# Optimization experiments

Hardware: AMD Instinct MI355X
Metric: run time of the kernel (lower is better)

Reference implementation:

```python
import jax, jax.numpy as jnp
import numpy as np
import math

D_MODEL = 1024
NUM_HEADS = 16
BATCH = 2
SEQ = 2048

def setup_inputs() -> dict:
    key = jax.random.key(0)
    ks = jax.random.split(key, 9)
    s = 1.0 / math.sqrt(D_MODEL)
    inp = {
        "X": jax.random.normal(ks[0], (BATCH, SEQ, D_MODEL), dtype=jnp.float32),
        "Wq": jax.random.uniform(ks[1], (D_MODEL, D_MODEL), jnp.float32, -s, s),
        "bq": jax.random.uniform(ks[2], (D_MODEL,), jnp.float32, -s, s),
        "Wk": jax.random.uniform(ks[3], (D_MODEL, D_MODEL), jnp.float32, -s, s),
        "bk": jax.random.uniform(ks[4], (D_MODEL,), jnp.float32, -s, s),
        "Wv": jax.random.uniform(ks[5], (D_MODEL, D_MODEL), jnp.float32, -s, s),
        "bv": jax.random.uniform(ks[6], (D_MODEL,), jnp.float32, -s, s),
        "Wo": jax.random.uniform(ks[7], (D_MODEL, D_MODEL), jnp.float32, -s, s),
        "bo": jax.random.uniform(ks[8], (D_MODEL,), jnp.float32, -s, s),
    }
    return inp

def reference(X, Wq, bq, Wk, bk, Wv, bv, Wo, bo):
    B, S, D = X.shape
    H = NUM_HEADS
    dk = D // H
    # QKV projections (Linear: x @ W.T + b; here W stored as [in, out] so x @ W + b)
    q = X @ Wq + bq
    k = X @ Wk + bk
    v = X @ Wv + bv
    # split heads -> [B, H, S, dk]
    q = q.reshape(B, S, H, dk).transpose(0, 2, 1, 3)
    k = k.reshape(B, S, H, dk).transpose(0, 2, 1, 3)
    v = v.reshape(B, S, H, dk).transpose(0, 2, 1, 3)
    scores = jnp.einsum("bhqd,bhkd->bhqk", q, k) / math.sqrt(dk)
    weights = jax.nn.softmax(scores, axis=-1)
    attn = jnp.einsum("bhqk,bhkd->bhqd", weights, v)
    concat = attn.transpose(0, 2, 1, 3).reshape(B, S, D)
    return concat @ Wo + bo
```

## Files before the change

kernel.cpp:

```cpp
#include <hip/hip_runtime.h>
#include <stdint.h>

#define D_MODEL 1024
#define NH      16
#define DKH     64
#define BATCH   2
#define SEQ     2048
#define M_TOK   (BATCH*SEQ)

typedef __attribute__((ext_vector_type(8))) short bf16x8;
typedef __attribute__((ext_vector_type(4))) float f32x4;

__device__ __forceinline__ uint16_t f2b(float f) {
  uint32_t u = __builtin_bit_cast(uint32_t, f);
  return (uint16_t)((u + 0x7FFFu + ((u >> 16) & 1u)) >> 16);
}

__device__ __forceinline__ void gl2lds16(const uint16_t* g, uint16_t* l) {
  __builtin_amdgcn_global_load_lds(
      (const __attribute__((address_space(1))) void*)g,
      (__attribute__((address_space(3))) void*)l, 16, 0, 0);
}

__global__ void convx(const float* __restrict__ X, uint16_t* __restrict__ Xb) {
  int i = (blockIdx.x * 256 + threadIdx.x) * 8;
  float4 a = *(const float4*)(X + i);
  float4 b = *(const float4*)(X + i + 4);
  uint16_t tmp[8] = {f2b(a.x), f2b(a.y), f2b(a.z), f2b(a.w),
                     f2b(b.x), f2b(b.y), f2b(b.z), f2b(b.w)};
  *(uint4*)(Xb + i) = *(const uint4*)tmp;
}

__global__ void wtrans(const float* __restrict__ W0, const float* __restrict__ W1,
                       const float* __restrict__ W2, const float* __restrict__ W3,
                       uint16_t* __restrict__ T0, uint16_t* __restrict__ T1,
                       uint16_t* __restrict__ T2, uint16_t* __restrict__ T3) {
  __shared__ float tile[32][33];
  int z = blockIdx.z;
  const float* W = (z == 0) ? W0 : (z == 1) ? W1 : (z == 2) ? W2 : W3;
  uint16_t*    T = (z == 0) ? T0 : (z == 1) ? T1 : (z == 2) ? T2 : T3;
  int k0 = blockIdx.x * 32, n0 = blockIdx.y * 32;
  int tx = threadIdx.x, ty = threadIdx.y;
  tile[ty][tx] = W[(size_t)(k0 + ty) * D_MODEL + n0 + tx];
  __syncthreads();
  T[(size_t)(n0 + ty) * D_MODEL + k0 + tx] = f2b(tile[tx][ty]);
}

template <bool SWAP>
__device__ __forceinline__ void gemm_core(const uint16_t* __restrict__ A,
                                          const uint16_t* __restrict__ BT,
                                          uint16_t* As, uint16_t* Bs,
                                          int m0, int n0, int kBeg, int kEnd,
                                          f32x4 (&acc)[4][4]) {
  const int t    = threadIdx.x;
  const int lane = t & 63;
  const int qi   = lane & 15, g = lane >> 4;
  const int wm   = (t >> 7) & 1;
  const int wn   = (t >> 6) & 1;
  const int srow = t >> 2;
  const int sc   = (t & 3) ^ ((t >> 3) & 3);
  const int wbase = t & 192;
  const int rch  = (g ^ ((qi >> 1) & 3)) * 8;

  const uint16_t* Ag = A  + (size_t)(m0 + srow) * D_MODEL + sc * 8;
  const uint16_t* Bg = BT + (size_t)(n0 + srow) * D_MODEL + sc * 8;

#pragma unroll
  for (int j = 0; j < 2; j++) {
    gl2lds16(Ag + (size_t)j * 64 * D_MODEL + kBeg, As + (j * 256 + wbase) * 8);
    gl2lds16(Bg + (size_t)j * 64 * D_MODEL + kBeg, Bs + (j * 256 + wbase) * 8);
  }

  int cur = 0;
  for (int k0 = kBeg; k0 < kEnd; k0 += 32) {
    __syncthreads();
    int kn = k0 + 32;
    if (kn < kEnd) {
      int nb = (cur ^ 1) * 4096;
#pragma unroll
      for (int j = 0; j < 2; j++) {
        gl2lds16(Ag + (size_t)j * 64 * D_MODEL + kn, As + nb + (j * 256 + wbase) * 8);
        gl2lds16(Bg + (size_t)j * 64 * D_MODEL + kn, Bs + nb + (j * 256 + wbase) * 8);
      }
    }
    const uint16_t* Ab = As + cur * 4096;
    const uint16_t* Bb = Bs + cur * 4096;
    bf16x8 af[4], bf[4];
#pragma unroll
    for (int i = 0; i < 4; i++) {
      af[i] = *(const bf16x8*)(Ab + (wm * 64 + i * 16 + qi) * 32 + rch);
      bf[i] = *(const bf16x8*)(Bb + (wn * 64 + i * 16 + qi) * 32 + rch);
    }
#pragma unroll
    for (int i = 0; i < 4; i++)
#pragma unroll
      for (int j = 0; j < 4; j++)
        acc[i][j] = SWAP
          ? __builtin_amdgcn_mfma_f32_16x16x32_bf16(bf[j], af[i], acc[i][j], 0, 0, 0)
          : __builtin_amdgcn_mfma_f32_16x16x32_bf16(af[i], bf[j], acc[i][j], 0, 0, 0);
    cur ^= 1;
  }
}

__global__ __launch_bounds__(256) void qkv_gemm(
    const uint16_t* __restrict__ Xb,
    const uint16_t* __restrict__ WqT, const uint16_t* __restrict__ WkT,
    const uint16_t* __restrict__ WvT,
    const float* __restrict__ bq, const float* __restrict__ bk,
    const float* __restrict__ bv,
    uint16_t* __restrict__ Qo, uint16_t* __restrict__ Ko, uint16_t* __restrict__ Vt) {
  __shared__ __align__(16) uint16_t smem[17408];
  uint16_t* As = smem;
  uint16_t* Bs = smem + 8192;
  uint16_t* T  = smem;
  const int z = blockIdx.z;
  const uint16_t* BT  = (z == 0) ? WqT : (z == 1) ? WkT : WvT;
  const float*   bias = (z == 0) ? bq  : (z == 1) ? bk  : bv;
  const int m0 = blockIdx.y * 128, n0 = blockIdx.x * 128;
  const int lane = threadIdx.x & 63, qi = lane & 15, g = lane >> 4;
  const int wm = (threadIdx.x >> 7) & 1, wn = (threadIdx.x >> 6) & 1;
  const float l2e = 1.4426950408889634f * 0.125f;

  const f32x4 ZERO = {0.f, 0.f, 0.f, 0.f};
  f32x4 acc[4][4];
#pragma unroll
  for (int i = 0; i < 4; i++)
#pragma unroll
    for (int j = 0; j < 4; j++) acc[i][j] = ZERO;

  if (z == 2) {
    gemm_core<false>(Xb, BT, As, Bs, m0, n0, 0, D_MODEL, acc);
    __syncthreads();
#pragma unroll
    for (int i = 0; i < 4; i++) {
      int tok = wm * 64 + i * 16 + g * 4;
#pragma unroll
      for (int j = 0; j < 4; j++) {
        int ch = wn * 64 + j * 16 + qi;
        float bb = bias[n0 + ch];
        uint32_t lo = (uint32_t)f2b(acc[i][j][0] + bb) | ((uint32_t)f2b(acc[i][j][1] + bb) << 16);
        uint32_t hi = (uint32_t)f2b(acc[i][j][2] + bb) | ((uint32_t)f2b(acc[i][j][3] + bb) << 16);
        uint2 pk = {lo, hi};
        *(uint2*)(T + ch * 136 + tok) = pk;
      }
    }
    __syncthreads();
    {
      int ch = threadIdx.x >> 1, sh = threadIdx.x & 1;
      const uint16_t* src = T + ch * 136 + sh * 64;
      int bidx = m0 >> 11;
      uint16_t* dst = Vt + ((size_t)(bidx * D_MODEL + n0 + ch)) * SEQ + (m0 & 2047) + sh * 64;
#pragma unroll
      for (int u = 0; u < 8; u++)
        *(uint4*)(dst + u * 8) = *(const uint4*)(src + u * 8);
    }
  } else {
    gemm_core<true>(Xb, BT, As, Bs, m0, n0, 0, D_MODEL, acc);
    uint16_t* O = z ? Ko : Qo;
    const float osc = (z == 0) ? l2e : 1.0f;
#pragma unroll
    for (int i = 0; i < 4; i++) {
      size_t tok = m0 + wm * 64 + i * 16 + qi;
#pragma unroll
      for (int j = 0; j < 4; j++) {
        int ch = n0 + wn * 64 + j * 16 + g * 4;
        float4 bb = *(const float4*)(bias + ch);
        uint32_t lo = (uint32_t)f2b((acc[i][j][0] + bb.x) * osc) |
                      ((uint32_t)f2b((acc[i][j][1] + bb.y) * osc) << 16);
        uint32_t hi = (uint32_t)f2b((acc[i][j][2] + bb.z) * osc) |
                      ((uint32_t)f2b((acc[i][j][3] + bb.w) * osc) << 16);
        uint2 pk = {lo, hi};
        *(uint2*)(O + tok * D_MODEL + ch) = pk;
      }
    }
  }
}

__global__ __launch_bounds__(256) void oproj_gemm(
    const uint16_t* __restrict__ Ab, const uint16_t* __restrict__ WoT,
    const float* __restrict__ bo, float* __restrict__ out) {
  __shared__ __align__(16) uint16_t As[8192];
  __shared__ __align__(16) uint16_t Bs[4096];
  const int t = threadIdx.x;
  const int lane = t & 63, qi = lane & 15, g = lane >> 4;
  const int wm = (t >> 7) & 1;
  const int wn = (t >> 6) & 1;
  const int srow = t >> 2;
  const int sc = (t & 3) ^ ((t >> 3) & 3);
  const int wbase = t & 192;
  const int rch = (g ^ ((qi >> 1) & 3)) * 8;
  const int m0 = blockIdx.y * 128, n0 = blockIdx.x * 64;

  const uint16_t* Ag = Ab  + (size_t)(m0 + srow) * D_MODEL + sc * 8;
  const uint16_t* Bg = WoT + (size_t)(n0 + srow) * D_MODEL + sc * 8;

  const f32x4 ZERO = {0.f, 0.f, 0.f, 0.f};
  f32x4 acc[4][2];
#pragma unroll
  for (int i = 0; i < 4; i++)
#pragma unroll
    for (int j = 0; j < 2; j++) acc[i][j] = ZERO;

  gl2lds16(Ag, As + wbase * 8);
  gl2lds16(Ag + (size_t)64 * D_MODEL, As + (256 + wbase) * 8);
  gl2lds16(Bg, Bs + wbase * 8);

  int cur = 0;
  for (int k0 = 0; k0 < D_MODEL; k0 += 32) {
    __syncthreads();
    int kn = k0 + 32;
    if (kn < D_MODEL) {
      int nbA = (cur ^ 1) * 4096, nbB = (cur ^ 1) * 2048;
      gl2lds16(Ag + kn, As + nbA + wbase * 8);
      gl2lds16(Ag + (size_t)64 * D_MODEL + kn, As + nbA + (256 + wbase) * 8);
      gl2lds16(Bg + kn, Bs + nbB + wbase * 8);
    }
    const uint16_t* Abuf = As + cur * 4096;
    const uint16_t* Bbuf = Bs + cur * 2048;
    bf16x8 af[4], bf[2];
#pragma unroll
    for (int i = 0; i < 4; i++)
      af[i] = *(const bf16x8*)(Abuf + (wm * 64 + i * 16 + qi) * 32 + rch);
#pragma unroll
    for (int j = 0; j < 2; j++)
      bf[j] = *(const bf16x8*)(Bbuf + (wn * 32 + j * 16 + qi) * 32 + rch);
#pragma unroll
    for (int i = 0; i < 4; i++)
#pragma unroll
      for (int j = 0; j < 2; j++)
        acc[i][j] = __builtin_amdgcn_mfma_f32_16x16x32_bf16(bf[j], af[i], acc[i][j], 0, 0, 0);
    cur ^= 1;
  }

#pragma unroll
  for (int i = 0; i < 4; i++) {
    size_t tok = m0 + wm * 64 + i * 16 + qi;
#pragma unroll
    for (int j = 0; j < 2; j++) {
      int ch = n0 + wn * 32 + j * 16 + g * 4;
      float4 bb = *(const float4*)(bo + ch);
      float4 o = {acc[i][j][0] + bb.x, acc[i][j][1] + bb.y,
                  acc[i][j][2] + bb.z, acc[i][j][3] + bb.w};
      *(float4*)(out + tok * D_MODEL + ch) = o;
    }
  }
}

__global__ __launch_bounds__(256) void attn_fwd(
    const uint16_t* __restrict__ Q, const uint16_t* __restrict__ K,
    const uint16_t* __restrict__ Vt, uint16_t* __restrict__ O) {
  __shared__ __align__(16) uint16_t sm[24576];
  uint16_t* Ps = sm + 16384;

  const int t = threadIdx.x, lane = t & 63, w = t >> 6;
  const int g = lane >> 4, qi = lane & 15;
  const int wbase = t & 192;
  const int sc = (t & 3) ^ ((t >> 3) & 3);
  const int rch = (g ^ ((qi >> 1) & 3)) * 8;
  const int key = qi & 7;
  const int q0 = blockIdx.x * 128;
  const int bh = blockIdx.y, b = bh >> 4, h = bh & 15;
  const uint16_t* Qp = Q + (size_t)b * SEQ * D_MODEL + h * DKH;
  const uint16_t* Kp = K + (size_t)b * SEQ * D_MODEL + h * DKH;
  const uint16_t* Vp = Vt + (size_t)bh * DKH * SEQ;

  const int srow = t >> 2, c8 = sc * 8;

#pragma unroll
  for (int hs = 0; hs < 2; hs++)
#pragma unroll
    for (int j = 0; j < 2; j++)
      gl2lds16(Qp + (size_t)(q0 + j * 64 + srow) * D_MODEL + hs * 32 + c8,
               sm + 16384 + hs * 4096 + (j * 256 + wbase) * 8);
  {
    const uint16_t* Kr = Kp + (size_t)srow * D_MODEL;
    const uint16_t* Vr = Vp + (size_t)srow * SEQ;
    gl2lds16(Kr + c8,      sm + wbase * 8);
    gl2lds16(Kr + 32 + c8, sm + 2048 + wbase * 8);
    gl2lds16(Vr + c8,      sm + 8192 + wbase * 8);
    gl2lds16(Vr + 32 + c8, sm + 8192 + 2048 + wbase * 8);
  }
  __syncthreads();

  bf16x8 qf[2][2];
#pragma unroll
  for (int ks = 0; ks < 2; ks++)
#pragma unroll
    for (int i = 0; i < 2; i++)
      qf[ks][i] = *(const bf16x8*)(sm + 16384 + ks * 4096 + (w * 32 + i * 16 + qi) * 32 + rch);
  __syncthreads();

  float lsum[2] = {0.f, 0.f};
  const f32x4 ZERO = {0.f, 0.f, 0.f, 0.f};
  f32x4 oaccT[4][2];
#pragma unroll
  for (int d = 0; d < 4; d++)
#pragma unroll
    for (int i = 0; i < 2; i++) oaccT[d][i] = ZERO;

  int cur = 0;
  for (int kt = 0; kt < SEQ / 64; kt++) {
    if (kt + 1 < SEQ / 64) {
      int nb = (cur ^ 1) * 4096;
      const uint16_t* Kr = Kp + (size_t)((kt + 1) * 64 + srow) * D_MODEL;
      const uint16_t* Vr = Vp + (size_t)srow * SEQ + (kt + 1) * 64;
      gl2lds16(Kr + c8,      sm + nb + wbase * 8);
      gl2lds16(Kr + 32 + c8, sm + nb + 2048 + wbase * 8);
      gl2lds16(Vr + c8,      sm + 8192 + nb + wbase * 8);
      gl2lds16(Vr + 32 + c8, sm + 8192 + nb + 2048 + wbase * 8);
    }
    const uint16_t* Kb = sm + cur * 4096;
    const uint16_t* Vb = sm + 8192 + cur * 4096;

    f32x4 sacc[4][2];
#pragma unroll
    for (int j = 0; j < 4; j++)
#pragma unroll
      for (int i = 0; i < 2; i++) sacc[j][i] = ZERO;
#pragma unroll
    for (int ks = 0; ks < 2; ks++) {
      const uint16_t* Ksb = Kb + ks * 2048;
      bf16x8 kf[4];
#pragma unroll
      for (int j = 0; j < 4; j++)
        kf[j] = *(const bf16x8*)(Ksb + (j * 16 + qi) * 32 + rch);
#pragma unroll
      for (int j = 0; j < 4; j++)
#pragma unroll
        for (int i = 0; i < 2; i++)
          sacc[j][i] = __builtin_amdgcn_mfma_f32_16x16x32_bf16(kf[j], qf[ks][i], sacc[j][i], 0, 0, 0);
    }

#pragma unroll
    for (int i = 0; i < 2; i++) {
      uint16_t* Pr = Ps + (w * 32 + i * 16 + qi) * 64;
#pragma unroll
      for (int j = 0; j < 4; j++) {
        float p0 = __builtin_amdgcn_exp2f(sacc[j][i][0]);
        float p1 = __builtin_amdgcn_exp2f(sacc[j][i][1]);
        float p2 = __builtin_amdgcn_exp2f(sacc[j][i][2]);
        float p3 = __builtin_amdgcn_exp2f(sacc[j][i][3]);
        lsum[i] += (p0 + p1) + (p2 + p3);
        uint2 pk = {__builtin_amdgcn_perm(__builtin_bit_cast(uint32_t, p1),
                                          __builtin_bit_cast(uint32_t, p0), 0x07060302u),
                    __builtin_amdgcn_perm(__builtin_bit_cast(uint32_t, p3),
                                          __builtin_bit_cast(uint32_t, p2), 0x07060302u)};
        *(uint2*)(Pr + (((j * 4 + g) ^ (2 * key)) << 2)) = pk;
      }
    }

#pragma unroll
    for (int ks = 0; ks < 2; ks++) {
      const uint16_t* Vsb = Vb + ks * 2048;
      bf16x8 vf[4], pf[2];
#pragma unroll
      for (int d = 0; d < 4; d++)
        vf[d] = *(const bf16x8*)(Vsb + (d * 16 + qi) * 32 + rch);
#pragma unroll
      for (int i = 0; i < 2; i++)
        pf[i] = *(const bf16x8*)(Ps + (w * 32 + i * 16 + qi) * 64 +
                                 (((ks * 4 + g) ^ key) << 3));
#pragma unroll
      for (int d = 0; d < 4; d++)
#pragma unroll
        for (int i = 0; i < 2; i++)
          oaccT[d][i] = __builtin_amdgcn_mfma_f32_16x16x32_bf16(vf[d], pf[i], oaccT[d][i], 0, 0, 0);
    }

    if (kt + 1 < SEQ / 64) __syncthreads();
    cur ^= 1;
  }

#pragma unroll
  for (int i = 0; i < 2; i++) {
    lsum[i] += __shfl_xor(lsum[i], 16, 64);
    lsum[i] += __shfl_xor(lsum[i], 32, 64);
  }
  float rl[2] = {1.f / lsum[0], 1.f / lsum[1]};

#pragma unroll
  for (int i = 0; i < 2; i++) {
    size_t row = (size_t)b * SEQ + q0 + w * 32 + i * 16 + qi;
#pragma unroll
    for (int d = 0; d < 4; d++) {
      uint32_t lo = (uint32_t)f2b(oaccT[d][i][0] * rl[i]) |
                    ((uint32_t)f2b(oaccT[d][i][1] * rl[i]) << 16);
      uint32_t hi = (uint32_t)f2b(oaccT[d][i][2] * rl[i]) |
                    ((uint32_t)f2b(oaccT[d][i][3] * rl[i]) << 16);
      uint2 pk = {lo, hi};
      *(uint2*)(O + row * D_MODEL + h * DKH + d * 16 + g * 4) = pk;
    }
  }
}

extern "C" void kernel_launch(void* const* d_in, const int* in_sizes, int n_in,
                              void* d_out, int out_size, void* d_ws, size_t ws_size,
                              hipStream_t stream) {
  (void)in_sizes; (void)n_in; (void)out_size; (void)ws_size;
  const float* X  = (const float*)d_in[0];
  const float* Wq = (const float*)d_in[1];
  const float* bq = (const float*)d_in[2];
  const float* Wk = (const float*)d_in[3];
  const float* bk = (const float*)d_in[4];
  const float* Wv = (const float*)d_in[5];
  const float* bv = (const float*)d_in[6];
  const float* Wo = (const float*)d_in[7];
  const float* bo = (const float*)d_in[8];
  float* out = (float*)d_out;

  char* p = (char*)d_ws;
  uint16_t* Xb  = (uint16_t*)p; p += (size_t)M_TOK * D_MODEL * 2;
  uint16_t* WqT = (uint16_t*)p; p += (size_t)D_MODEL * D_MODEL * 2;
  uint16_t* WkT = (uint16_t*)p; p += (size_t)D_MODEL * D_MODEL * 2;
  uint16_t* WvT = (uint16_t*)p; p += (size_t)D_MODEL * D_MODEL * 2;
  uint16_t* WoT = (uint16_t*)p; p += (size_t)D_MODEL * D_MODEL * 2;
  uint16_t* Qw  = (uint16_t*)p; p += (size_t)M_TOK * D_MODEL * 2;
  uint16_t* Kw  = (uint16_t*)p; p += (size_t)M_TOK * D_MODEL * 2;
  uint16_t* Vt  = (uint16_t*)p; p += (size_t)M_TOK * D_MODEL * 2;
  uint16_t* Ob  = (uint16_t*)p; p += (size_t)M_TOK * D_MODEL * 2;

  convx<<<(M_TOK * D_MODEL) / (256 * 8), 256, 0, stream>>>(X, Xb);
  wtrans<<<dim3(32, 32, 4), dim3(32, 32), 0, stream>>>(Wq, Wk, Wv, Wo, WqT, WkT, WvT, WoT);
  qkv_gemm<<<dim3(8, 32, 3), 256, 0, stream>>>(Xb, WqT, WkT, WvT, bq, bk, bv, Qw, Kw, Vt);
  attn_fwd<<<dim3(SEQ / 128, BATCH * NH), 256, 0, stream>>>(Qw, Kw, Vt, Ob);
  oproj_gemm<<<dim3(16, 32), 256, 0, stream>>>(Ob, WoT, bo, out);
}
```

Before: 203.9 us.

## Split attention over key halves with combine kernel; narrow QKV GEMM tiles

Attention is split into two key-range halves along a new grid dimension. Each half writes unnormalized fp32 partial outputs and row sums, and a new combine kernel adds them, normalizes and writes bf16. The QKV GEMM switches to a shared 128x64 tile routine, doubling its block count. This raises parallelism and occupancy, at the cost of extra fp32 partial traffic, an added launch, and reliance on the softmax not needing per-split max rescaling.

```diff
diff --git a/kernel.cpp b/kernel.cpp
--- a/kernel.cpp
+++ b/kernel.cpp
@@ -47,11 +47,10 @@
 }
 
 template <bool SWAP>
-__device__ __forceinline__ void gemm_core(const uint16_t* __restrict__ A,
-                                          const uint16_t* __restrict__ BT,
-                                          uint16_t* As, uint16_t* Bs,
-                                          int m0, int n0, int kBeg, int kEnd,
-                                          f32x4 (&acc)[4][4]) {
+__device__ __forceinline__ void gemm64(const uint16_t* __restrict__ A,
+                                       const uint16_t* __restrict__ BT,
+                                       uint16_t* As, uint16_t* Bs,
+                                       int m0, int n0, f32x4 (&acc)[4][2]) {
   const int t    = threadIdx.x;
   const int lane = t & 63;
   const int qi   = lane & 15, g = lane >> 4;
@@ -65,142 +64,6 @@
   const uint16_t* Ag = A  + (size_t)(m0 + srow) * D_MODEL + sc * 8;
   const uint16_t* Bg = BT + (size_t)(n0 + srow) * D_MODEL + sc * 8;
 
-#pragma unroll
-  for (int j = 0; j < 2; j++) {
-    gl2lds16(Ag + (size_t)j * 64 * D_MODEL + kBeg, As + (j * 256 + wbase) * 8);
-    gl2lds16(Bg + (size_t)j * 64 * D_MODEL + kBeg, Bs + (j * 256 + wbase) * 8);
-  }
-
-  int cur = 0;
-  for (int k0 = kBeg; k0 < kEnd; k0 += 32) {
-    __syncthreads();
-    int kn = k0 + 32;
-    if (kn < kEnd) {
-      int nb = (cur ^ 1) * 4096;
-#pragma unroll
-      for (int j = 0; j < 2; j++) {
-        gl2lds16(Ag + (size_t)j * 64 * D_MODEL + kn, As + nb + (j * 256 + wbase) * 8);
-        gl2lds16(Bg + (size_t)j * 64 * D_MODEL + kn, Bs + nb + (j * 256 + wbase) * 8);
-      }
-    }
-    const uint16_t* Ab = As + cur * 4096;
-    const uint16_t* Bb = Bs + cur * 4096;
-    bf16x8 af[4], bf[4];
-#pragma unroll
-    for (int i = 0; i < 4; i++) {
-      af[i] = *(const bf16x8*)(Ab + (wm * 64 + i * 16 + qi) * 32 + rch);
-      bf[i] = *(const bf16x8*)(Bb + (wn * 64 + i * 16 + qi) * 32 + rch);
-    }
-#pragma unroll
-    for (int i = 0; i < 4; i++)
-#pragma unroll
-      for (int j = 0; j < 4; j++)
-        acc[i][j] = SWAP
-          ? __builtin_amdgcn_mfma_f32_16x16x32_bf16(bf[j], af[i], acc[i][j], 0, 0, 0)
-          : __builtin_amdgcn_mfma_f32_16x16x32_bf16(af[i], bf[j], acc[i][j], 0, 0, 0);
-    cur ^= 1;
-  }
-}
-
-__global__ __launch_bounds__(256) void qkv_gemm(
-    const uint16_t* __restrict__ Xb,
-    const uint16_t* __restrict__ WqT, const uint16_t* __restrict__ WkT,
-    const uint16_t* __restrict__ WvT,
-    const float* __restrict__ bq, const float* __restrict__ bk,
-    const float* __restrict__ bv,
-    uint16_t* __restrict__ Qo, uint16_t* __restrict__ Ko, uint16_t* __restrict__ Vt) {
-  __shared__ __align__(16) uint16_t smem[17408];
-  uint16_t* As = smem;
-  uint16_t* Bs = smem + 8192;
-  uint16_t* T  = smem;
-  const int z = blockIdx.z;
-  const uint16_t* BT  = (z == 0) ? WqT : (z == 1) ? WkT : WvT;
-  const float*   bias = (z == 0) ? bq  : (z == 1) ? bk  : bv;
-  const int m0 = blockIdx.y * 128, n0 = blockIdx.x * 128;
-  const int lane = threadIdx.x & 63, qi = lane & 15, g = lane >> 4;
-  const int wm = (threadIdx.x >> 7) & 1, wn = (threadIdx.x >> 6) & 1;
-  const float l2e = 1.4426950408889634f * 0.125f;
-
-  const f32x4 ZERO = {0.f, 0.f, 0.f, 0.f};
-  f32x4 acc[4][4];
-#pragma unroll
-  for (int i = 0; i < 4; i++)
-#pragma unroll
-    for (int j = 0; j < 4; j++) acc[i][j] = ZERO;
-
-  if (z == 2) {
-    gemm_core<false>(Xb, BT, As, Bs, m0, n0, 0, D_MODEL, acc);
-    __syncthreads();
-#pragma unroll
-    for (int i = 0; i < 4; i++) {
-      int tok = wm * 64 + i * 16 + g * 4;
-#pragma unroll
-      for (int j = 0; j < 4; j++) {
-        int ch = wn * 64 + j * 16 + qi;
-        float bb = bias[n0 + ch];
-        uint32_t lo = (uint32_t)f2b(acc[i][j][0] + bb) | ((uint32_t)f2b(acc[i][j][1] + bb) << 16);
-        uint32_t hi = (uint32_t)f2b(acc[i][j][2] + bb) | ((uint32_t)f2b(acc[i][j][3] + bb) << 16);
-        uint2 pk = {lo, hi};
-        *(uint2*)(T + ch * 136 + tok) = pk;
-      }
-    }
-    __syncthreads();
-    {
-      int ch = threadIdx.x >> 1, sh = threadIdx.x & 1;
-      const uint16_t* src = T + ch * 136 + sh * 64;
-      int bidx = m0 >> 11;
-      uint16_t* dst = Vt + ((size_t)(bidx * D_MODEL + n0 + ch)) * SEQ + (m0 & 2047) + sh * 64;
-#pragma unroll
-      for (int u = 0; u < 8; u++)
-        *(uint4*)(dst + u * 8) = *(const uint4*)(src + u * 8);
-    }
-  } else {
-    gemm_core<true>(Xb, BT, As, Bs, m0, n0, 0, D_MODEL, acc);
-    uint16_t* O = z ? Ko : Qo;
-    const float osc = (z == 0) ? l2e : 1.0f;
-#pragma unroll
-    for (int i = 0; i < 4; i++) {
-      size_t tok = m0 + wm * 64 + i * 16 + qi;
-#pragma unroll
-      for (int j = 0; j < 4; j++) {
-        int ch = n0 + wn * 64 + j * 16 + g * 4;
-        float4 bb = *(const float4*)(bias + ch);
-        uint32_t lo = (uint32_t)f2b((acc[i][j][0] + bb.x) * osc) |
-                      ((uint32_t)f2b((acc[i][j][1] + bb.y) * osc) << 16);
-        uint32_t hi = (uint32_t)f2b((acc[i][j][2] + bb.z) * osc) |
-                      ((uint32_t)f2b((acc[i][j][3] + bb.w) * osc) << 16);
-        uint2 pk = {lo, hi};
-        *(uint2*)(O + tok * D_MODEL + ch) = pk;
-      }
-    }
-  }
-}
-
-__global__ __launch_bounds__(256) void oproj_gemm(
-    const uint16_t* __restrict__ Ab, const uint16_t* __restrict__ WoT,
-    const float* __restrict__ bo, float* __restrict__ out) {
-  __shared__ __align__(16) uint16_t As[8192];
-  __shared__ __align__(16) uint16_t Bs[4096];
-  const int t = threadIdx.x;
-  const int lane = t & 63, qi = lane & 15, g = lane >> 4;
-  const int wm = (t >> 7) & 1;
-  const int wn = (t >> 6) & 1;
-  const int srow = t >> 2;
-  const int sc = (t & 3) ^ ((t >> 3) & 3);
-  const int wbase = t & 192;
-  const int rch = (g ^ ((qi >> 1) & 3)) * 8;
-  const int m0 = blockIdx.y * 128, n0 = blockIdx.x * 64;
-
-  const uint16_t* Ag = Ab  + (size_t)(m0 + srow) * D_MODEL + sc * 8;
-  const uint16_t* Bg = WoT + (size_t)(n0 + srow) * D_MODEL + sc * 8;
-
-  const f32x4 ZERO = {0.f, 0.f, 0.f, 0.f};
-  f32x4 acc[4][2];
-#pragma unroll
-  for (int i = 0; i < 4; i++)
-#pragma unroll
-    for (int j = 0; j < 2; j++) acc[i][j] = ZERO;
-
   gl2lds16(Ag, As + wbase * 8);
   gl2lds16(Ag + (size_t)64 * D_MODEL, As + (256 + wbase) * 8);
   gl2lds16(Bg, Bs + wbase * 8);
@@ -215,22 +78,116 @@
       gl2lds16(Ag + (size_t)64 * D_MODEL + kn, As + nbA + (256 + wbase) * 8);
       gl2lds16(Bg + kn, Bs + nbB + wbase * 8);
     }
-    const uint16_t* Abuf = As + cur * 4096;
-    const uint16_t* Bbuf = Bs + cur * 2048;
+    const uint16_t* Ab = As + cur * 4096;
+    const uint16_t* Bb = Bs + cur * 2048;
     bf16x8 af[4], bf[2];
 #pragma unroll
     for (int i = 0; i < 4; i++)
-      af[i] = *(const bf16x8*)(Abuf + (wm * 64 + i * 16 + qi) * 32 + rch);
+      af[i] = *(const bf16x8*)(Ab + (wm * 64 + i * 16 + qi) * 32 + rch);
 #pragma unroll
     for (int j = 0; j < 2; j++)
-      bf[j] = *(const bf16x8*)(Bbuf + (wn * 32 + j * 16 + qi) * 32 + rch);
+      bf[j] = *(const bf16x8*)(Bb + (wn * 32 + j * 16 + qi) * 32 + rch);
 #pragma unroll
     for (int i = 0; i < 4; i++)
 #pragma unroll
       for (int j = 0; j < 2; j++)
-        acc[i][j] = __builtin_amdgcn_mfma_f32_16x16x32_bf16(bf[j], af[i], acc[i][j], 0, 0, 0);
+        acc[i][j] = SWAP
+          ? __builtin_amdgcn_mfma_f32_16x16x32_bf16(bf[j], af[i], acc[i][j], 0, 0, 0)
+          : __builtin_amdgcn_mfma_f32_16x16x32_bf16(af[i], bf[j], acc[i][j], 0, 0, 0);
     cur ^= 1;
   }
+}
+
+__global__ __launch_bounds__(256) void qkv_gemm(
+    const uint16_t* __restrict__ Xb,
+    const uint16_t* __restrict__ WqT, const uint16_t* __restrict__ WkT,
+    const uint16_t* __restrict__ WvT,
+    const float* __restrict__ bq, const float* __restrict__ bk,
+    const float* __restrict__ bv,
+    uint16_t* __restrict__ Qo, uint16_t* __restrict__ Ko, uint16_t* __restrict__ Vt) {
+  __shared__ __align__(16) uint16_t smem[12288];
+  uint16_t* As = smem;
+  uint16_t* Bs = smem + 8192;
+  uint16_t* T  = smem;
+  const int z = blockIdx.z;
+  const uint16_t* BT  = (z == 0) ? WqT : (z == 1) ? WkT : WvT;
+  const float*   bias = (z == 0) ? bq  : (z == 1) ? bk  : bv;
+  const int m0 = blockIdx.y * 128, n0 = blockIdx.x * 64;
+  const int lane = threadIdx.x & 63, qi = lane & 15, g = lane >> 4;
+  const int wm = (threadIdx.x >> 7) & 1, wn = (threadIdx.x >> 6) & 1;
+  const float l2e = 1.4426950408889634f * 0.125f;
+
+  const f32x4 ZERO = {0.f, 0.f, 0.f, 0.f};
+  f32x4 acc[4][2];
+#pragma unroll
+  for (int i = 0; i < 4; i++)
+#pragma unroll
+    for (int j = 0; j < 2; j++) acc[i][j] = ZERO;
+
+  if (z == 2) {
+    gemm64<false>(Xb, BT, As, Bs, m0, n0, acc);
+    __syncthreads();
+#pragma unroll
+    for (int i = 0; i < 4; i++) {
+      int tok = wm * 64 + i * 16 + g * 4;
+#pragma unroll
+      for (int j = 0; j < 2; j++) {
+        int ch = wn * 32 + j * 16 + qi;
+        float bb = bias[n0 + ch];
+        uint32_t lo = (uint32_t)f2b(acc[i][j][0] + bb) | ((uint32_t)f2b(acc[i][j][1] + bb) << 16);
+        uint32_t hi = (uint32_t)f2b(acc[i][j][2] + bb) | ((uint32_t)f2b(acc[i][j][3] + bb) << 16);
+        uint2 pk = {lo, hi};
+        *(uint2*)(T + ch * 136 + tok) = pk;
+      }
+    }
+    __syncthreads();
+    {
+      int ch = threadIdx.x >> 2, sh = threadIdx.x & 3;
+      const uint16_t* src = T + ch * 136 + sh * 32;
+      int bidx = m0 >> 11;
+      uint16_t* dst = Vt + ((size_t)(bidx * D_MODEL + n0 + ch)) * SEQ + (m0 & 2047) + sh * 32;
+#pragma unroll
+      for (int u = 0; u < 4; u++)
+        *(uint4*)(dst + u * 8) = *(const uint4*)(src + u * 8);
+    }
+  } else {
+    gemm64<true>(Xb, BT, As, Bs, m0, n0, acc);
+    uint16_t* O = z ? Ko : Qo;
+    const float osc = (z == 0) ? l2e : 1.0f;
+#pragma unroll
+    for (int i = 0; i < 4; i++) {
+      size_t tok = m0 + wm * 64 + i * 16 + qi;
+#pragma unroll
+      for (int j = 0; j < 2; j++) {
+        int ch = n0 + wn * 32 + j * 16 + g * 4;
+        float4 bb = *(const float4*)(bias + ch);
+        uint32_t lo = (uint32_t)f2b((acc[i][j][0] + bb.x) * osc) |
+                      ((uint32_t)f2b((acc[i][j][1] + bb.y) * osc) << 16);
+        uint32_t hi = (uint32_t)f2b((acc[i][j][2] + bb.z) * osc) |
+                      ((uint32_t)f2b((acc[i][j][3] + bb.w) * osc) << 16);
+        uint2 pk = {lo, hi};
+        *(uint2*)(O + tok * D_MODEL + ch) = pk;
+      }
+    }
+  }
+}
+
+__global__ __launch_bounds__(256) void oproj_gemm(
+    const uint16_t* __restrict__ Ab, const uint16_t* __restrict__ WoT,
+    const float* __restrict__ bo, float* __restrict__ out) {
+  __shared__ __align__(16) uint16_t As[8192];
+  __shared__ __align__(16) uint16_t Bs[4096];
+  const int m0 = blockIdx.y * 128, n0 = blockIdx.x * 64;
+  const int lane = threadIdx.x & 63, qi = lane & 15, g = lane >> 4;
+  const int wm = (threadIdx.x >> 7) & 1, wn = (threadIdx.x >> 6) & 1;
+  const f32x4 ZERO = {0.f, 0.f, 0.f, 0.f};
+  f32x4 acc[4][2];
+#pragma unroll
+  for (int i = 0; i < 4; i++)
+#pragma unroll
+    for (int j = 0; j < 2; j++) acc[i][j] = ZERO;
+
+  gemm64<true>(Ab, WoT, As, Bs, m0, n0, acc);
 
 #pragma unroll
   for (int i = 0; i < 4; i++) {
@@ -248,7 +205,8 @@
 
 __global__ __launch_bounds__(256) void attn_fwd(
     const uint16_t* __restrict__ Q, const uint16_t* __restrict__ K,
-    const uint16_t* __restrict__ Vt, uint16_t* __restrict__ O) {
+    const uint16_t* __restrict__ Vt,
+    float* __restrict__ P0, float* __restrict__ P1, float* __restrict__ lw) {
   __shared__ __align__(16) uint16_t sm[24576];
   uint16_t* Ps = sm + 16384;
 
@@ -258,8 +216,10 @@
   const int sc = (t & 3) ^ ((t >> 3) & 3);
   const int rch = (g ^ ((qi >> 1) & 3)) * 8;
   const int key = qi & 7;
-  const int q0 = blockIdx.x * 128;
+  const int qt = blockIdx.x, q0 = qt * 128;
   const int bh = blockIdx.y, b = bh >> 4, h = bh & 15;
+  const int kz = blockIdx.z;
+  const int ktBeg = kz * 16, ktEnd = ktBeg + 16;
   const uint16_t* Qp = Q + (size_t)b * SEQ * D_MODEL + h * DKH;
   const uint16_t* Kp = K + (size_t)b * SEQ * D_MODEL + h * DKH;
   const uint16_t* Vp = Vt + (size_t)bh * DKH * SEQ;
@@ -273,8 +233,8 @@
       gl2lds16(Qp + (size_t)(q0 + j * 64 + srow) * D_MODEL + hs * 32 + c8,
                sm + 16384 + hs * 4096 + (j * 256 + wbase) * 8);
   {
-    const uint16_t* Kr = Kp + (size_t)srow * D_MODEL;
-    const uint16_t* Vr = Vp + (size_t)srow * SEQ;
+    const uint16_t* Kr = Kp + (size_t)(ktBeg * 64 + srow) * D_MODEL;
+    const uint16_t* Vr = Vp + (size_t)srow * SEQ + ktBeg * 64;
     gl2lds16(Kr + c8,      sm + wbase * 8);
     gl2lds16(Kr + 32 + c8, sm + 2048 + wbase * 8);
     gl2lds16(Vr + c8,      sm + 8192 + wbase * 8);
@@ -299,8 +259,8 @@
     for (int i = 0; i < 2; i++) oaccT[d][i] = ZERO;
 
   int cur = 0;
-  for (int kt = 0; kt < SEQ / 64; kt++) {
-    if (kt + 1 < SEQ / 64) {
+  for (int kt = ktBeg; kt < ktEnd; kt++) {
+    if (kt + 1 < ktEnd) {
       int nb = (cur ^ 1) * 4096;
       const uint16_t* Kr = Kp + (size_t)((kt + 1) * 64 + srow) * D_MODEL;
       const uint16_t* Vr = Vp + (size_t)srow * SEQ + (kt + 1) * 64;
@@ -367,7 +327,7 @@
           oaccT[d][i] = __builtin_amdgcn_mfma_f32_16x16x32_bf16(vf[d], pf[i], oaccT[d][i], 0, 0, 0);
     }
 
-    if (kt + 1 < SEQ / 64) __syncthreads();
+    if (kt + 1 < ktEnd) __syncthreads();
     cur ^= 1;
   }
 
@@ -376,20 +336,42 @@
     lsum[i] += __shfl_xor(lsum[i], 16, 64);
     lsum[i] += __shfl_xor(lsum[i], 32, 64);
   }
-  float rl[2] = {1.f / lsum[0], 1.f / lsum[1]};
-
+  if (lane < 16) {
+    float* lp = lw + ((size_t)kz * 512 + bh * 16 + qt) * 128;
+#pragma unroll
+    for (int i = 0; i < 2; i++) lp[w * 32 + i * 16 + qi] = lsum[i];
+  }
+
+  float* Pout = (kz ? P1 : P0) + ((size_t)(bh * 16 + qt) * 128) * 64;
 #pragma unroll
   for (int i = 0; i < 2; i++) {
-    size_t row = (size_t)b * SEQ + q0 + w * 32 + i * 16 + qi;
-#pragma unroll
-    for (int d = 0; d < 4; d++) {
-      uint32_t lo = (uint32_t)f2b(oaccT[d][i][0] * rl[i]) |
-                    ((uint32_t)f2b(oaccT[d][i][1] * rl[i]) << 16);
-      uint32_t hi = (uint32_t)f2b(oaccT[d][i][2] * rl[i]) |
-                    ((uint32_t)f2b(oaccT[d][i][3] * rl[i]) << 16);
-      uint2 pk = {lo, hi};
-      *(uint2*)(O + row * D_MODEL + h * DKH + d * 16 + g * 4) = pk;
-    }
+    int q = w * 32 + i * 16 + qi;
+#pragma unroll
+    for (int d = 0; d < 4; d++)
+      *(f32x4*)(Pout + q * 64 + d * 16 + g * 4) = oaccT[d][i];
+  }
+}
+
+__global__ __launch_bounds__(256) void attn_combine(
+    const float* __restrict__ P0, const float* __restrict__ P1,
+    const float* __restrict__ lw, uint16_t* __restrict__ Ob) {
+  const int c = blockIdx.x;
+  const int bh = c >> 4, qt = c & 15;
+  const int b = bh >> 4, h = bh & 15;
+  const int t = threadIdx.x;
+  const int q = t >> 1, dh = (t & 1) * 32;
+  const float l = lw[(size_t)c * 128 + q] + lw[65536 + (size_t)c * 128 + q];
+  const float rl = 1.f / l;
+  const size_t base = ((size_t)c * 128 + q) * 64 + dh;
+  uint16_t* dst = Ob + ((size_t)(b * SEQ + qt * 128 + q)) * D_MODEL + h * DKH + dh;
+#pragma unroll
+  for (int u = 0; u < 8; u++) {
+    float4 a = *(const float4*)(P0 + base + u * 4);
+    float4 v = *(const float4*)(P1 + base + u * 4);
+    uint32_t lo = (uint32_t)f2b((a.x + v.x) * rl) | ((uint32_t)f2b((a.y + v.y) * rl) << 16);
+    uint32_t hi = (uint32_t)f2b((a.z + v.z) * rl) | ((uint32_t)f2b((a.w + v.w) * rl) << 16);
+    uint2 pk = {lo, hi};
+    *(uint2*)(dst + u * 4) = pk;
   }
 }
 
@@ -418,10 +400,14 @@
   uint16_t* Kw  = (uint16_t*)p; p += (size_t)M_TOK * D_MODEL * 2;
   uint16_t* Vt  = (uint16_t*)p; p += (size_t)M_TOK * D_MODEL * 2;
   uint16_t* Ob  = (uint16_t*)p; p += (size_t)M_TOK * D_MODEL * 2;
+  float*    P1  = (float*)p;    p += (size_t)M_TOK * D_MODEL * 4;
+  float*    lw  = (float*)p;    p += (size_t)2 * M_TOK * NH * 4;
+  float*    P0  = out;
 
   convx<<<(M_TOK * D_MODEL) / (256 * 8), 256, 0, stream>>>(X, Xb);
   wtrans<<<dim3(32, 32, 4), dim3(32, 32), 0, stream>>>(Wq, Wk, Wv, Wo, WqT, WkT, WvT, WoT);
-  qkv_gemm<<<dim3(8, 32, 3), 256, 0, stream>>>(Xb, WqT, WkT, WvT, bq, bk, bv, Qw, Kw, Vt);
-  attn_fwd<<<dim3(SEQ / 128, BATCH * NH), 256, 0, stream>>>(Qw, Kw, Vt, Ob);
+  qkv_gemm<<<dim3(16, 32, 3), 256, 0, stream>>>(Xb, WqT, WkT, WvT, bq, bk, bv, Qw, Kw, Vt);
+  attn_fwd<<<dim3(16, 32, 2), 256, 0, stream>>>(Qw, Kw, Vt, P0, P1, lw);
+  attn_combine<<<512, 256, 0, stream>>>(P0, P1, lw, Ob);
   oproj_gemm<<<dim3(16, 32), 256, 0, stream>>>(Ob, WoT, bo, out);
 }
```

Measured after the change: 232.4 us. 1.14x slower.

## Halve attention query tile to 64 rows and load Q straight into registers

Applied to the files above, without the earlier changes.

Each attention block now handles 64 queries instead of 128, with every wave owning 16 query rows, so the grid has twice as many blocks. Launch bounds are raised to 4 blocks per CU and the LDS footprint is trimmed. Q fragments are read from global memory directly into registers instead of being staged through LDS, which removes one barrier. The GEMM helpers are also refactored to drop unused k-range parameters and share an oproj core. The aim is better CU occupancy and latency hiding, at the cost of reading each K/V tile twice as often and getting less MFMA reuse per LDS load.

```diff
diff --git a/kernel.cpp b/kernel.cpp
--- a/kernel.cpp
+++ b/kernel.cpp
@@ -50,8 +50,7 @@
 __device__ __forceinline__ void gemm_core(const uint16_t* __restrict__ A,
                                           const uint16_t* __restrict__ BT,
                                           uint16_t* As, uint16_t* Bs,
-                                          int m0, int n0, int kBeg, int kEnd,
-                                          f32x4 (&acc)[4][4]) {
+                                          int m0, int n0, f32x4 (&acc)[4][4]) {
   const int t    = threadIdx.x;
   const int lane = t & 63;
   const int qi   = lane & 15, g = lane >> 4;
@@ -67,15 +66,15 @@
 
 #pragma unroll
   for (int j = 0; j < 2; j++) {
-    gl2lds16(Ag + (size_t)j * 64 * D_MODEL + kBeg, As + (j * 256 + wbase) * 8);
-    gl2lds16(Bg + (size_t)j * 64 * D_MODEL + kBeg, Bs + (j * 256 + wbase) * 8);
+    gl2lds16(Ag + (size_t)j * 64 * D_MODEL, As + (j * 256 + wbase) * 8);
+    gl2lds16(Bg + (size_t)j * 64 * D_MODEL, Bs + (j * 256 + wbase) * 8);
   }
 
   int cur = 0;
-  for (int k0 = kBeg; k0 < kEnd; k0 += 32) {
+  for (int k0 = 0; k0 < D_MODEL; k0 += 32) {
     __syncthreads();
     int kn = k0 + 32;
-    if (kn < kEnd) {
+    if (kn < D_MODEL) {
       int nb = (cur ^ 1) * 4096;
 #pragma unroll
       for (int j = 0; j < 2; j++) {
@@ -98,6 +97,55 @@
         acc[i][j] = SWAP
           ? __builtin_amdgcn_mfma_f32_16x16x32_bf16(bf[j], af[i], acc[i][j], 0, 0, 0)
           : __builtin_amdgcn_mfma_f32_16x16x32_bf16(af[i], bf[j], acc[i][j], 0, 0, 0);
+    cur ^= 1;
+  }
+}
+
+__device__ __forceinline__ void gemm64(const uint16_t* __restrict__ A,
+                                       const uint16_t* __restrict__ BT,
+                                       uint16_t* As, uint16_t* Bs,
+                                       int m0, int n0, f32x4 (&acc)[4][2]) {
+  const int t    = threadIdx.x;
+  const int lane = t & 63;
+  const int qi   = lane & 15, g = lane >> 4;
+  const int wm   = (t >> 7) & 1;
+  const int wn   = (t >> 6) & 1;
+  const int srow = t >> 2;
+  const int sc   = (t & 3) ^ ((t >> 3) & 3);
+  const int wbase = t & 192;
+  const int rch  = (g ^ ((qi >> 1) & 3)) * 8;
+
+  const uint16_t* Ag = A  + (size_t)(m0 + srow) * D_MODEL + sc * 8;
+  const uint16_t* Bg = BT + (size_t)(n0 + srow) * D_MODEL + sc * 8;
+
+  gl2lds16(Ag, As + wbase * 8);
+  gl2lds16(Ag + (size_t)64 * D_MODEL, As + (256 + wbase) * 8);
+  gl2lds16(Bg, Bs + wbase * 8);
+
+  int cur = 0;
+  for (int k0 = 0; k0 < D_MODEL; k0 += 32) {
+    __syncthreads();
+    int kn = k0 + 32;
+    if (kn < D_MODEL) {
+      int nbA = (cur ^ 1) * 4096, nbB = (cur ^ 1) * 2048;
+      gl2lds16(Ag + kn, As + nbA + wbase * 8);
+      gl2lds16(Ag + (size_t)64 * D_MODEL + kn, As + nbA + (256 + wbase) * 8);
+      gl2lds16(Bg + kn, Bs + nbB + wbase * 8);
+    }
+    const uint16_t* Ab = As + cur * 4096;
+    const uint16_t* Bb = Bs + cur * 2048;
+    bf16x8 af[4], bf[2];
+#pragma unroll
+    for (int i = 0; i < 4; i++)
+      af[i] = *(const bf16x8*)(Ab + (wm * 64 + i * 16 + qi) * 32 + rch);
+#pragma unroll
+    for (int j = 0; j < 2; j++)
+      bf[j] = *(const bf16x8*)(Bb + (wn * 32 + j * 16 + qi) * 32 + rch);
+#pragma unroll
+    for (int i = 0; i < 4; i++)
+#pragma unroll
+      for (int j = 0; j < 2; j++)
+        acc[i][j] = __builtin_amdgcn_mfma_f32_16x16x32_bf16(bf[j], af[i], acc[i][j], 0, 0, 0);
     cur ^= 1;
   }
 }
@@ -129,7 +177,7 @@
     for (int j = 0; j < 4; j++) acc[i][j] = ZERO;
 
   if (z == 2) {
-    gemm_core<false>(Xb, BT, As, Bs, m0, n0, 0, D_MODEL, acc);
+    gemm_core<false>(Xb, BT, As, Bs, m0, n0, acc);
     __syncthreads();
 #pragma unroll
     for (int i = 0; i < 4; i++) {
@@ -155,7 +203,7 @@
         *(uint4*)(dst + u * 8) = *(const uint4*)(src + u * 8);
     }
   } else {
-    gemm_core<true>(Xb, BT, As, Bs, m0, n0, 0, D_MODEL, acc);
+    gemm_core<true>(Xb, BT, As, Bs, m0, n0, acc);
     uint16_t* O = z ? Ko : Qo;
     const float osc = (z == 0) ? l2e : 1.0f;
 #pragma unroll
@@ -181,19 +229,9 @@
     const float* __restrict__ bo, float* __restrict__ out) {
   __shared__ __align__(16) uint16_t As[8192];
   __shared__ __align__(16) uint16_t Bs[4096];
-  const int t = threadIdx.x;
-  const int lane = t & 63, qi = lane & 15, g = lane >> 4;
-  const int wm = (t >> 7) & 1;
-  const int wn = (t >> 6) & 1;
-  const int srow = t >> 2;
-  const int sc = (t & 3) ^ ((t >> 3) & 3);
-  const int wbase = t & 192;
-  const int rch = (g ^ ((qi >> 1) & 3)) * 8;
   const int m0 = blockIdx.y * 128, n0 = blockIdx.x * 64;
-
-  const uint16_t* Ag = Ab  + (size_t)(m0 + srow) * D_MODEL + sc * 8;
-  const uint16_t* Bg = WoT + (size_t)(n0 + srow) * D_MODEL + sc * 8;
-
+  const int lane = threadIdx.x & 63, qi = lane & 15, g = lane >> 4;
+  const int wm = (threadIdx.x >> 7) & 1, wn = (threadIdx.x >> 6) & 1;
   const f32x4 ZERO = {0.f, 0.f, 0.f, 0.f};
   f32x4 acc[4][2];
 #pragma unroll
@@ -201,36 +239,7 @@
 #pragma unroll
     for (int j = 0; j < 2; j++) acc[i][j] = ZERO;
 
-  gl2lds16(Ag, As + wbase * 8);
-  gl2lds16(Ag + (size_t)64 * D_MODEL, As + (256 + wbase) * 8);
-  gl2lds16(Bg, Bs + wbase * 8);
-
-  int cur = 0;
-  for (int k0 = 0; k0 < D_MODEL; k0 += 32) {
-    __syncthreads();
-    int kn = k0 + 32;
-    if (kn < D_MODEL) {
-      int nbA = (cur ^ 1) * 4096, nbB = (cur ^ 1) * 2048;
-      gl2lds16(Ag + kn, As + nbA + wbase * 8);
-      gl2lds16(Ag + (size_t)64 * D_MODEL + kn, As + nbA + (256 + wbase) * 8);
-      gl2lds16(Bg + kn, Bs + nbB + wbase * 8);
-    }
-    const uint16_t* Abuf = As + cur * 4096;
-    const uint16_t* Bbuf = Bs + cur * 2048;
-    bf16x8 af[4], bf[2];
-#pragma unroll
-    for (int i = 0; i < 4; i++)
-      af[i] = *(const bf16x8*)(Abuf + (wm * 64 + i * 16 + qi) * 32 + rch);
-#pragma unroll
-    for (int j = 0; j < 2; j++)
-      bf[j] = *(const bf16x8*)(Bbuf + (wn * 32 + j * 16 + qi) * 32 + rch);
-#pragma unroll
-    for (int i = 0; i < 4; i++)
-#pragma unroll
-      for (int j = 0; j < 2; j++)
-        acc[i][j] = __builtin_amdgcn_mfma_f32_16x16x32_bf16(bf[j], af[i], acc[i][j], 0, 0, 0);
-    cur ^= 1;
-  }
+  gemm64(Ab, WoT, As, Bs, m0, n0, acc);
 
 #pragma unroll
   for (int i = 0; i < 4; i++) {
@@ -246,10 +255,10 @@
   }
 }
 
-__global__ __launch_bounds__(256) void attn_fwd(
+__global__ __launch_bounds__(256, 4) void attn_fwd(
     const uint16_t* __restrict__ Q, const uint16_t* __restrict__ K,
     const uint16_t* __restrict__ Vt, uint16_t* __restrict__ O) {
-  __shared__ __align__(16) uint16_t sm[24576];
+  __shared__ __align__(16) uint16_t sm[20480];
   uint16_t* Ps = sm + 16384;
 
   const int t = threadIdx.x, lane = t & 63, w = t >> 6;
@@ -258,20 +267,13 @@
   const int sc = (t & 3) ^ ((t >> 3) & 3);
   const int rch = (g ^ ((qi >> 1) & 3)) * 8;
   const int key = qi & 7;
-  const int q0 = blockIdx.x * 128;
+  const int q0 = blockIdx.x * 64;
   const int bh = blockIdx.y, b = bh >> 4, h = bh & 15;
   const uint16_t* Qp = Q + (size_t)b * SEQ * D_MODEL + h * DKH;
   const uint16_t* Kp = K + (size_t)b * SEQ * D_MODEL + h * DKH;
   const uint16_t* Vp = Vt + (size_t)bh * DKH * SEQ;
-
   const int srow = t >> 2, c8 = sc * 8;
 
-#pragma unroll
-  for (int hs = 0; hs < 2; hs++)
-#pragma unroll
-    for (int j = 0; j < 2; j++)
-      gl2lds16(Qp + (size_t)(q0 + j * 64 + srow) * D_MODEL + hs * 32 + c8,
-               sm + 16384 + hs * 4096 + (j * 256 + wbase) * 8);
   {
     const uint16_t* Kr = Kp + (size_t)srow * D_MODEL;
     const uint16_t* Vr = Vp + (size_t)srow * SEQ;
@@ -280,23 +282,19 @@
     gl2lds16(Vr + c8,      sm + 8192 + wbase * 8);
     gl2lds16(Vr + 32 + c8, sm + 8192 + 2048 + wbase * 8);
   }
+  bf16x8 qf[2];
+  {
+    const uint16_t* qrow = Qp + (size_t)(q0 + w * 16 + qi) * D_MODEL + g * 8;
+    qf[0] = *(const bf16x8*)(qrow);
+    qf[1] = *(const bf16x8*)(qrow + 32);
+  }
   __syncthreads();
 
-  bf16x8 qf[2][2];
-#pragma unroll
-  for (int ks = 0; ks < 2; ks++)
-#pragma unroll
-    for (int i = 0; i < 2; i++)
-      qf[ks][i] = *(const bf16x8*)(sm + 16384 + ks * 4096 + (w * 32 + i * 16 + qi) * 32 + rch);
-  __syncthreads();
-
-  float lsum[2] = {0.f, 0.f};
+  float lsum = 0.f;
   const f32x4 ZERO = {0.f, 0.f, 0.f, 0.f};
-  f32x4 oaccT[4][2];
-#pragma unroll
-  for (int d = 0; d < 4; d++)
-#pragma unroll
-    for (int i = 0; i < 2; i++) oaccT[d][i] = ZERO;
+  f32x4 oaccT[4];
+#pragma unroll
+  for (int d = 0; d < 4; d++) oaccT[d] = ZERO;
 
   int cur = 0;
   for (int kt = 0; kt < SEQ / 64; kt++) {
@@ -312,11 +310,9 @@
     const uint16_t* Kb = sm + cur * 4096;
     const uint16_t* Vb = sm + 8192 + cur * 4096;
 
-    f32x4 sacc[4][2];
-#pragma unroll
-    for (int j = 0; j < 4; j++)
-#pragma unroll
-      for (int i = 0; i < 2; i++) sacc[j][i] = ZERO;
+    f32x4 sacc[4];
+#pragma unroll
+    for (int j = 0; j < 4; j++) sacc[j] = ZERO;
 #pragma unroll
     for (int ks = 0; ks < 2; ks++) {
       const uint16_t* Ksb = Kb + ks * 2048;
@@ -326,21 +322,18 @@
         kf[j] = *(const bf16x8*)(Ksb + (j * 16 + qi) * 32 + rch);
 #pragma unroll
       for (int j = 0; j < 4; j++)
-#pragma unroll
-        for (int i = 0; i < 2; i++)
-          sacc[j][i] = __builtin_amdgcn_mfma_f32_16x16x32_bf16(kf[j], qf[ks][i], sacc[j][i], 0, 0, 0);
-    }
-
-#pragma unroll
-    for (int i = 0; i < 2; i++) {
-      uint16_t* Pr = Ps + (w * 32 + i * 16 + qi) * 64;
+        sacc[j] = __builtin_amdgcn_mfma_f32_16x16x32_bf16(kf[j], qf[ks], sacc[j], 0, 0, 0);
+    }
+
+    {
+      uint16_t* Pr = Ps + (w * 16 + qi) * 64;
 #pragma unroll
       for (int j = 0; j < 4; j++) {
-        float p0 = __builtin_amdgcn_exp2f(sacc[j][i][0]);
-        float p1 = __builtin_amdgcn_exp2f(sacc[j][i][1]);
-        float p2 = __builtin_amdgcn_exp2f(sacc[j][i][2]);
-        float p3 = __builtin_amdgcn_exp2f(sacc[j][i][3]);
-        lsum[i] += (p0 + p1) + (p2 + p3);
+        float p0 = __builtin_amdgcn_exp2f(sacc[j][0]);
+        float p1 = __builtin_amdgcn_exp2f(sacc[j][1]);
+        float p2 = __builtin_amdgcn_exp2f(sacc[j][2]);
+        float p3 = __builtin_amdgcn_exp2f(sacc[j][3]);
+        lsum += (p0 + p1) + (p2 + p3);
         uint2 pk = {__builtin_amdgcn_perm(__builtin_bit_cast(uint32_t, p1),
                                           __builtin_bit_cast(uint32_t, p0), 0x07060302u),
                     __builtin_amdgcn_perm(__builtin_bit_cast(uint32_t, p3),
@@ -352,41 +345,32 @@
 #pragma unroll
     for (int ks = 0; ks < 2; ks++) {
       const uint16_t* Vsb = Vb + ks * 2048;
-      bf16x8 vf[4], pf[2];
+      bf16x8 vf[4], pf;
+      pf = *(const bf16x8*)(Ps + (w * 16 + qi) * 64 + (((ks * 4 + g) ^ key) << 3));
 #pragma unroll
       for (int d = 0; d < 4; d++)
         vf[d] = *(const bf16x8*)(Vsb + (d * 16 + qi) * 32 + rch);
 #pragma unroll
-      for (int i = 0; i < 2; i++)
-        pf[i] = *(const bf16x8*)(Ps + (w * 32 + i * 16 + qi) * 64 +
-                                 (((ks * 4 + g) ^ key) << 3));
-#pragma unroll
       for (int d = 0; d < 4; d++)
-#pragma unroll
-        for (int i = 0; i < 2; i++)
-          oaccT[d][i] = __builtin_amdgcn_mfma_f32_16x16x32_bf16(vf[d], pf[i], oaccT[d][i], 0, 0, 0);
+        oaccT[d] = __builtin_amdgcn_mfma_f32_16x16x32_bf16(vf[d], pf, oaccT[d], 0, 0, 0);
     }
 
     if (kt + 1 < SEQ / 64) __syncthreads();
     cur ^= 1;
   }
 
-#pragma unroll
-  for (int i = 0; i < 2; i++) {
-    lsum[i] += __shfl_xor(lsum[i], 16, 64);
-    lsum[i] += __shfl_xor(lsum[i], 32, 64);
-  }
-  float rl[2] = {1.f / lsum[0], 1.f / lsum[1]};
-
-#pragma unroll
-  for (int i = 0; i < 2; i++) {
-    size_t row = (size_t)b * SEQ + q0 + w * 32 + i * 16 + qi;
+  lsum += __shfl_xor(lsum, 16, 64);
+  lsum += __shfl_xor(lsum, 32, 64);
+  float rl = 1.f / lsum;
+
+  {
+    size_t row = (size_t)b * SEQ + q0 + w * 16 + qi;
 #pragma unroll
     for (int d = 0; d < 4; d++) {
-      uint32_t lo = (uint32_t)f2b(oaccT[d][i][0] * rl[i]) |
-                    ((uint32_t)f2b(oaccT[d][i][1] * rl[i]) << 16);
-      uint32_t hi = (uint32_t)f2b(oaccT[d][i][2] * rl[i]) |
-                    ((uint32_t)f2b(oaccT[d][i][3] * rl[i]) << 16);
+      uint32_t lo = (uint32_t)f2b(oaccT[d][0] * rl) |
+                    ((uint32_t)f2b(oaccT[d][1] * rl) << 16);
+      uint32_t hi = (uint32_t)f2b(oaccT[d][2] * rl) |
+                    ((uint32_t)f2b(oaccT[d][3] * rl) << 16);
       uint2 pk = {lo, hi};
       *(uint2*)(O + row * D_MODEL + h * DKH + d * 16 + g * 4) = pk;
     }
@@ -422,6 +406,6 @@
   convx<<<(M_TOK * D_MODEL) / (256 * 8), 256, 0, stream>>>(X, Xb);
   wtrans<<<dim3(32, 32, 4), dim3(32, 32), 0, stream>>>(Wq, Wk, Wv, Wo, WqT, WkT, WvT, WoT);
   qkv_gemm<<<dim3(8, 32, 3), 256, 0, stream>>>(Xb, WqT, WkT, WvT, bq, bk, bv, Qw, Kw, Vt);
-  attn_fwd<<<dim3(SEQ / 128, BATCH * NH), 256, 0, stream>>>(Qw, Kw, Vt, Ob);
+  attn_fwd<<<dim3(SEQ / 64, BATCH * NH), 256, 0, stream>>>(Qw, Kw, Vt, Ob);
   oproj_gemm<<<dim3(16, 32), 256, 0, stream>>>(Ob, WoT, bo, out);
 }
```

Result: no change. 205.7 us (+0.9%).
